# Performance work log

Measured on AMD Instinct MI355X. Metric: run time of the kernel, lower is better.

Reference implementation:

```python
import jax, jax.numpy as jnp
import numpy as np

N_NODES = 100000
E_HALF = 2000000  # edges come in two mirrored halves (two classes per node pair)
IN_DIM, HID = 5, 16


def setup_inputs() -> dict:
    key = jax.random.key(0)
    ks = jax.random.split(key, 8)
    x = jax.random.normal(ks[0], (N_NODES, IN_DIM), dtype=jnp.float32)
    e_half = jax.random.randint(ks[1], (2, E_HALF), 0, N_NODES)
    edges = jnp.concatenate([e_half, e_half], axis=1)  # [2, 2*E_HALF]
    edge_attr = jax.random.uniform(ks[2], (2 * E_HALF, 2), dtype=jnp.float32)
    detector_labels = jax.random.bernoulli(ks[3], 0.5, (N_NODES,))
    s = 1.0 / np.sqrt(IN_DIM)
    W_rel = jax.random.uniform(ks[4], (HID, IN_DIM), minval=-s, maxval=s, dtype=jnp.float32)
    b_rel = jax.random.uniform(ks[5], (HID,), minval=-s, maxval=s, dtype=jnp.float32)
    W_root = jax.random.uniform(ks[6], (HID, IN_DIM), minval=-s, maxval=s, dtype=jnp.float32)
    s2 = 1.0 / np.sqrt(2 * HID + 1)
    k7, k8 = jax.random.split(ks[7])
    W_lin = jax.random.uniform(k7, (1, 2 * HID + 1), minval=-s2, maxval=s2, dtype=jnp.float32)
    b_lin = jax.random.uniform(k8, (1,), minval=-s2, maxval=s2, dtype=jnp.float32)
    return {
        "x": x, "edges": edges, "edge_attr": edge_attr,
        "detector_labels": detector_labels,
        "W_rel": W_rel, "b_rel": b_rel, "W_root": W_root,
        "W_lin": W_lin, "b_lin": b_lin,
    }


def reference(x, edges, edge_attr, detector_labels, W_rel, b_rel, W_root, W_lin, b_lin):
    N = x.shape[0]
    src, dst = edges[0], edges[1]
    # GraphConv(aggr='add'): out_i = W_root x_i + W_rel * sum_{(j->i)} w_e * x_j + b_rel
    w = edge_attr[:, 1]
    msg = x[src] * w[:, None]                                  # [E, 5]
    agg = jax.ops.segment_sum(msg, dst, num_segments=N)        # [N, 5]
    h = jnp.tanh(agg @ W_rel.T + b_rel + x @ W_root.T)         # [N, 16]
    # SplitSyndromes: keep edges whose both endpoints are detector nodes
    valid = detector_labels[src] & detector_labels[dst]
    vidx = jnp.nonzero(valid)[0]                               # data-dependent (eager)
    e = edges[:, vidx]
    ea = edge_attr[vidx]
    # gather-concat-linear edge scoring
    feat = jnp.concatenate([h[e[0]], ea[:, :1], h[e[1]]], axis=-1)  # [nv, 33]
    score = feat @ W_lin.T + b_lin                             # [nv, 1]
    nv = score.shape[0]
    half = nv // 2
    score2 = score.reshape(-1, half)                           # [2, half]
    classes2 = ea[:, 1].reshape(-1, half)
    mi = jnp.argmin(score2, axis=0)
    cols = jnp.arange(half)
    return e[:, :half], score2[mi, cols], classes2[mi, cols]
```

## Files before the change

### kernel.cpp

```cpp
#include <hip/hip_runtime.h>

#define HID 16
#define IN_DIM 5
#define PAD 8
#define EPT 4

#define FXS 64.0f
#define FXI 0.015625f

__global__ void pack_labels(const int* __restrict__ lab, const float* __restrict__ x,
                            unsigned long long* __restrict__ bits, float* __restrict__ xp,
                            int N) {
    int n = blockIdx.x * 256 + threadIdx.x;
    bool p = (n < N) && (lab[n] != 0);
    unsigned long long m = __ballot(p);
    if (((threadIdx.x & 63) == 0) && n < N) bits[n >> 6] = m;
    if (n < N) {
        float4 a;
        a.x = x[(size_t)n * IN_DIM + 0];
        a.y = x[(size_t)n * IN_DIM + 1];
        a.z = x[(size_t)n * IN_DIM + 2];
        a.w = x[(size_t)n * IN_DIM + 3];
        *(float4*)(xp + (size_t)n * 8) = a;
        float4 b;
        b.x = x[(size_t)n * IN_DIM + 4];
        b.y = 0.f; b.z = 0.f; b.w = 0.f;
        *(float4*)(xp + (size_t)n * 8 + 4) = b;
    }
}

__global__ __launch_bounds__(256, 4) void scatter_count(
        const int* __restrict__ src, const int* __restrict__ dst,
        const unsigned long long* __restrict__ bits,
        const float2* __restrict__ ea2,
        const float* __restrict__ xp,
        const float* __restrict__ Wlin,
        unsigned long long* __restrict__ agg,
        int* __restrict__ counts,
        float4* __restrict__ st4,
        int EH) {
    const int tid = threadIdx.x;
    const int i0 = (blockIdx.x * 256 + tid) * EPT;

    int s[EPT], d[EPT];
    float2 eaA[EPT], eaB[EPT];
    bool act[EPT];

    if (i0 + EPT <= EH && ((EH & 1) == 0)) {
        int4 s4 = *(const int4*)(src + i0);
        int4 d4 = *(const int4*)(dst + i0);
        s[0] = s4.x; s[1] = s4.y; s[2] = s4.z; s[3] = s4.w;
        d[0] = d4.x; d[1] = d4.y; d[2] = d4.z; d[3] = d4.w;
        float4 a0 = *(const float4*)(ea2 + i0);
        float4 a1 = *(const float4*)(ea2 + i0 + 2);
        float4 b0 = *(const float4*)(ea2 + (size_t)i0 + EH);
        float4 b1 = *(const float4*)(ea2 + (size_t)i0 + EH + 2);
        eaA[0] = make_float2(a0.x, a0.y); eaA[1] = make_float2(a0.z, a0.w);
        eaA[2] = make_float2(a1.x, a1.y); eaA[3] = make_float2(a1.z, a1.w);
        eaB[0] = make_float2(b0.x, b0.y); eaB[1] = make_float2(b0.z, b0.w);
        eaB[2] = make_float2(b1.x, b1.y); eaB[3] = make_float2(b1.z, b1.w);
#pragma unroll
        for (int k = 0; k < EPT; k++) act[k] = true;
    } else {
#pragma unroll
        for (int k = 0; k < EPT; k++) {
            int i = i0 + k;
            act[k] = (i < EH);
            s[k] = act[k] ? src[i] : 0;
            d[k] = act[k] ? dst[i] : 0;
            eaA[k] = act[k] ? ea2[i] : make_float2(0.f, 0.f);
            eaB[k] = act[k] ? ea2[(size_t)i + EH] : make_float2(0.f, 0.f);
        }
    }

    bool ld[EPT], vl[EPT];
#pragma unroll
    for (int k = 0; k < EPT; k++) {
        bool ls = (bits[s[k] >> 6] >> (s[k] & 63)) & 1;
        bool lv = (bits[d[k] >> 6] >> (d[k] & 63)) & 1;
        ld[k] = act[k] && lv;
        vl[k] = ld[k] && ls;
    }

    float4 xa[EPT], xb[EPT];
#pragma unroll
    for (int k = 0; k < EPT; k++) {
        const float* xs = xp + (size_t)s[k] * 8;
        xa[k] = *(const float4*)xs;
        xb[k] = *(const float4*)(xs + 4);
    }

#pragma unroll
    for (int k = 0; k < EPT; k++) {
        if (ld[k]) {
            float w = (eaA[k].y + eaB[k].y) * FXS;
            unsigned long long a = 0;
            int q0 = __float2int_rn(xa[k].x * w);
            int q1 = __float2int_rn(xa[k].y * w);
            int q2 = __float2int_rn(xa[k].z * w);
            int q3 = __float2int_rn(xa[k].w * w);
            int q4 = __float2int_rn(xb[k].x * w);
            a += (unsigned long long)(long long)q0;
            a += (unsigned long long)(long long)q1 << 12;
            a += (unsigned long long)(long long)q2 << 24;
            a += (unsigned long long)(long long)q3 << 36;
            a += (unsigned long long)(long long)q4 << 48;
            atomicAdd(&agg[(size_t)d[k] * PAD], a);
        }
    }

    float w16 = Wlin[HID];
    float scpart[EPT], cls[EPT];
#pragma unroll
    for (int k = 0; k < EPT; k++) {
        float p0 = w16 * eaA[k].x;
        float p1 = w16 * eaB[k].x;
        if (p1 < p0) { scpart[k] = p1; cls[k] = eaB[k].y; }
        else         { scpart[k] = p0; cls[k] = eaA[k].y; }
    }

    unsigned m4 = 0;
#pragma unroll
    for (int k = 0; k < EPT; k++) m4 |= (vl[k] ? (1u << k) : 0u);
    int cnt = __popc(m4);
    int lane = tid & 63, wid = tid >> 6;
    int scan = cnt;
#pragma unroll
    for (int off = 1; off < 64; off <<= 1) {
        int u = __shfl_up(scan, off, 64);
        if (lane >= off) scan += u;
    }
    __shared__ int wc[4];
    if (lane == 63) wc[wid] = scan;
    __syncthreads();
    if (tid == 0) counts[blockIdx.x] = wc[0] + wc[1] + wc[2] + wc[3];
    int wexcl = 0;
#pragma unroll
    for (int k = 0; k < 4; k++) if (k < wid) wexcl += wc[k];
    int idx = blockIdx.x * (256 * EPT) + wexcl + (scan - cnt);
#pragma unroll
    for (int k = 0; k < EPT; k++) {
        if (vl[k]) {
            float4 r;
            r.x = __int_as_float(s[k]);
            r.y = __int_as_float(d[k]);
            r.z = scpart[k];
            r.w = cls[k];
            st4[idx++] = r;
        }
    }
}

__device__ __forceinline__ float decode_field(unsigned long long& T) {
    int r = (int)(T & 0xFFFull);
    int s = (r >= 2048) ? r - 4096 : r;
    T = (T - (unsigned long long)(long long)s) >> 12;
    return (float)s * FXI;
}

__global__ void compute_uv(const float* __restrict__ xp,
                           const unsigned long long* __restrict__ agg,
                           const int* __restrict__ lab,
                           const float* __restrict__ Wrel, const float* __restrict__ brel,
                           const float* __restrict__ Wroot, const float* __restrict__ Wlin,
                           float2* __restrict__ uv, int N) {
    __shared__ float sWrel[HID * IN_DIM];
    __shared__ float sWroot[HID * IN_DIM];
    __shared__ float sBrel[HID];
    __shared__ float sWl[2 * HID + 1];
    int t = threadIdx.x;
    if (t < HID * IN_DIM) sWrel[t] = Wrel[t];
    else if (t < 2 * HID * IN_DIM) sWroot[t - HID * IN_DIM] = Wroot[t - HID * IN_DIM];
    else if (t < 2 * HID * IN_DIM + HID) sBrel[t - 2 * HID * IN_DIM] = brel[t - 2 * HID * IN_DIM];
    else if (t < 2 * HID * IN_DIM + HID + 2 * HID + 1)
        sWl[t - 2 * HID * IN_DIM - HID] = Wlin[t - 2 * HID * IN_DIM - HID];
    __syncthreads();

    int n = blockIdx.x * 256 + threadIdx.x;
    if (n >= N) return;
    if (!lab[n]) return;

    unsigned long long T = agg[(size_t)n * PAD];
    float a[IN_DIM], xv[IN_DIM];
#pragma unroll
    for (int d = 0; d < IN_DIM; d++) a[d] = decode_field(T);
    float4 x0 = *(const float4*)(xp + (size_t)n * 8);
    xv[0] = x0.x; xv[1] = x0.y; xv[2] = x0.z; xv[3] = x0.w;
    xv[4] = xp[(size_t)n * 8 + 4];

    float u = 0.f, vv = 0.f;
#pragma unroll
    for (int k = 0; k < HID; k++) {
        float acc = sBrel[k];
#pragma unroll
        for (int d = 0; d < IN_DIM; d++)
            acc += a[d] * sWrel[k * IN_DIM + d] + xv[d] * sWroot[k * IN_DIM + d];
        float hk = tanhf(acc);
        u += sWl[k] * hk;
        vv += sWl[HID + 1 + k] * hk;
    }
    uv[n] = make_float2(u, vv);
}

__global__ void scan_counts(const int* __restrict__ counts, int* __restrict__ offs, int nb) {
    __shared__ int waveSums[16];
    int tid = threadIdx.x;
    int base = tid * 8;
    int vals[8];
    int tsum = 0;
#pragma unroll
    for (int k = 0; k < 8; k++) {
        int idx = base + k;
        vals[k] = (idx < nb) ? counts[idx] : 0;
        tsum += vals[k];
    }
    int lane = tid & 63, wid = tid >> 6;
    int scan = tsum;
#pragma unroll
    for (int off = 1; off < 64; off <<= 1) {
        int u = __shfl_up(scan, off, 64);
        if (lane >= off) scan += u;
    }
    if (lane == 63) waveSums[wid] = scan;
    __syncthreads();
    if (wid == 0 && lane < 16) {
        int s = waveSums[lane];
#pragma unroll
        for (int off = 1; off < 16; off <<= 1) {
            int u = __shfl_up(s, off, 64);
            if (lane >= off) s += u;
        }
        waveSums[lane] = s;
    }
    __syncthreads();
    int waveBase = (wid > 0) ? waveSums[wid - 1] : 0;
    int excl = waveBase + scan - tsum;
#pragma unroll
    for (int k = 0; k < 8; k++) {
        int idx = base + k;
        if (idx < nb) offs[idx] = excl;
        excl += vals[k];
    }
}

__global__ void emit_out(const float4* __restrict__ st4,
                         const float* __restrict__ uvf, const float* __restrict__ blin,
                         const int* __restrict__ counts, const int* __restrict__ offs,
                         float* __restrict__ out, int K) {
    int b = blockIdx.x;
    int cnt = counts[b];
    int base = offs[b];
    float bl = blin[0];
    for (int t = threadIdx.x; t < cnt; t += 256) {
        float4 r = st4[(size_t)b * (256 * EPT) + t];
        int s = __float_as_int(r.x);
        int d = __float_as_int(r.y);
        float sc = bl + uvf[2 * (size_t)s] + uvf[2 * (size_t)d + 1] + r.z;
        int ro = base + t;
        out[ro] = (float)s;
        out[(size_t)K + ro] = (float)d;
        out[2 * (size_t)K + ro] = sc;
        out[3 * (size_t)K + ro] = r.w;
    }
}

extern "C" void kernel_launch(void* const* d_in, const int* in_sizes, int n_in,
                              void* d_out, int out_size, void* d_ws, size_t ws_size,
                              hipStream_t stream) {
    const float* x     = (const float*)d_in[0];
    const int*   edges = (const int*)d_in[1];
    const float* ea    = (const float*)d_in[2];
    const int*   lab   = (const int*)d_in[3];
    const float* Wrel  = (const float*)d_in[4];
    const float* brel  = (const float*)d_in[5];
    const float* Wroot = (const float*)d_in[6];
    const float* Wlin  = (const float*)d_in[7];
    const float* blin  = (const float*)d_in[8];

    const int N  = in_sizes[0] / IN_DIM;
    const int E  = in_sizes[1] / 2;
    const int EH = E / 2;
    const int K  = out_size / 4;

    const int* src = edges;
    const int* dst = edges + E;
    const float2* ea2 = (const float2*)ea;
    const int EPB = 256 * EPT;
    const int nb = (EH + EPB - 1) / EPB;
    const int nslots = nb * EPB;

    char* ws = (char*)d_ws;
    size_t off = 0;
    unsigned long long* agg = (unsigned long long*)(ws + off); off += (size_t)N * PAD * 8;
    float2* uv = (float2*)(ws + off); off += (size_t)N * 8;
    unsigned long long* bits = (unsigned long long*)(ws + off);
    off += (size_t)(((N + 63) / 64) * 8 + 255) / 256 * 256;
    float* xp = (float*)(ws + off); off += (size_t)N * 8 * 4;
    int* counts = (int*)(ws + off); off += (size_t)(nb * 4 + 255) / 256 * 256;
    int* offs   = (int*)(ws + off); off += (size_t)(nb * 4 + 255) / 256 * 256;
    float4* st4 = (float4*)(ws + off); off += (size_t)nslots * 16;

    float* out = (float*)d_out;

    hipMemsetAsync(agg, 0, (size_t)N * PAD * 8, stream);
    pack_labels<<<(N + 255) / 256, 256, 0, stream>>>(lab, x, bits, xp, N);
    scatter_count<<<nb, 256, 0, stream>>>(src, dst, bits, ea2, xp, Wlin, agg, counts,
                                          st4, EH);
    compute_uv<<<(N + 255) / 256, 256, 0, stream>>>(xp, agg, lab, Wrel, brel, Wroot, Wlin, uv, N);
    scan_counts<<<1, 1024, 0, stream>>>(counts, offs, nb);
    emit_out<<<nb, 256, 0, stream>>>(st4, (const float*)uv, blin, counts, offs, out, K);
}
```

Baseline: 178.3 us.

## Fuse all stages into one persistent kernel with grid-wide barriers

Replaces the memset-plus-five-kernel pipeline with a single persistent kernel. It walks the edge blocks in a grid-stride loop, scatters aggregates and compacts valid edges, then uses an atomic grid barrier before the block scan and per-node u/v compute, and a second barrier before the output emit. It also drops the label-bitmask and padded-x preprocessing and reads labels and unpadded x directly, loading x only for active edges. The aim is to remove launch gaps and the packing pass. In exchange it depends on every block being co-resident, sizes the grid from occupancy queries cached in a static, and the scan runs on a single block capped at 2048 edge blocks.

```diff
diff --git a/kernel.cpp b/kernel.cpp
--- a/kernel.cpp
+++ b/kernel.cpp
@@ -4,9 +4,241 @@
 #define IN_DIM 5
 #define PAD 8
 #define EPT 4
+#define EPB (256 * EPT)
 
 #define FXS 64.0f
 #define FXI 0.015625f
+
+__device__ __forceinline__ float decode_field(unsigned long long& T) {
+    int r = (int)(T & 0xFFFull);
+    int s = (r >= 2048) ? r - 4096 : r;
+    T = (T - (unsigned long long)(long long)s) >> 12;
+    return (float)s * FXI;
+}
+
+__device__ __forceinline__ void scan256(const int* __restrict__ counts,
+                                        int* __restrict__ offs, int nbv) {
+    __shared__ int wS[4];
+    int tid = threadIdx.x;
+    int base = tid * 8;
+    int vals[8];
+    int tsum = 0;
+#pragma unroll
+    for (int k = 0; k < 8; k++) {
+        int idx = base + k;
+        vals[k] = (idx < nbv) ? counts[idx] : 0;
+        tsum += vals[k];
+    }
+    int lane = tid & 63, wid = tid >> 6;
+    int scan = tsum;
+#pragma unroll
+    for (int off = 1; off < 64; off <<= 1) {
+        int u = __shfl_up(scan, off, 64);
+        if (lane >= off) scan += u;
+    }
+    if (lane == 63) wS[wid] = scan;
+    __syncthreads();
+    int waveBase = 0;
+#pragma unroll
+    for (int k = 0; k < 4; k++) if (k < wid) waveBase += wS[k];
+    int excl = waveBase + scan - tsum;
+#pragma unroll
+    for (int k = 0; k < 8; k++) {
+        int idx = base + k;
+        if (idx < nbv) offs[idx] = excl;
+        excl += vals[k];
+    }
+}
+
+__device__ __forceinline__ void gridbar(int* bar, int G) {
+    __syncthreads();
+    if (threadIdx.x == 0) {
+        __threadfence();
+        __hip_atomic_fetch_add(bar, 1, __ATOMIC_ACQ_REL, __HIP_MEMORY_SCOPE_AGENT);
+        while (__hip_atomic_load(bar, __ATOMIC_ACQUIRE, __HIP_MEMORY_SCOPE_AGENT) < G)
+            __builtin_amdgcn_s_sleep(32);
+        __threadfence();
+    }
+    __syncthreads();
+}
+
+__global__ __launch_bounds__(256) void fused(
+        const float* __restrict__ x, const int* __restrict__ src,
+        const int* __restrict__ dst, const float2* __restrict__ ea2,
+        const int* __restrict__ lab,
+        const float* __restrict__ Wrel, const float* __restrict__ brel,
+        const float* __restrict__ Wroot, const float* __restrict__ Wlin,
+        const float* __restrict__ blin,
+        unsigned long long* __restrict__ agg, float2* __restrict__ uvp,
+        int* __restrict__ counts, int* __restrict__ offs,
+        float4* __restrict__ st4, float* __restrict__ out,
+        int* __restrict__ bars,
+        int N, int EH, int K, int nbv) {
+    const int tid = threadIdx.x;
+    const int G = gridDim.x;
+    const int GT = G * 256;
+    const int gt = blockIdx.x * 256 + tid;
+    const int lane = tid & 63, wid = tid >> 6;
+
+    __shared__ float sWrel[HID * IN_DIM];
+    __shared__ float sWroot[HID * IN_DIM];
+    __shared__ float sBrel[HID];
+    __shared__ float sWl[2 * HID + 1];
+    if (tid < HID * IN_DIM) sWrel[tid] = Wrel[tid];
+    else if (tid < 2 * HID * IN_DIM) sWroot[tid - HID * IN_DIM] = Wroot[tid - HID * IN_DIM];
+    else if (tid < 2 * HID * IN_DIM + HID) sBrel[tid - 2 * HID * IN_DIM] = brel[tid - 2 * HID * IN_DIM];
+    else if (tid < 2 * HID * IN_DIM + HID + 2 * HID + 1)
+        sWl[tid - 2 * HID * IN_DIM - HID] = Wlin[tid - 2 * HID * IN_DIM - HID];
+
+    float w16 = Wlin[HID];
+    __shared__ int wc[4];
+    for (int vb = blockIdx.x; vb < nbv; vb += G) {
+        const int i0 = vb * EPB + tid * EPT;
+        int s[EPT], d[EPT];
+        float2 eaA[EPT], eaB[EPT];
+        bool act[EPT];
+        if (i0 + EPT <= EH) {
+            int4 s4 = *(const int4*)(src + i0);
+            int4 d4 = *(const int4*)(dst + i0);
+            s[0] = s4.x; s[1] = s4.y; s[2] = s4.z; s[3] = s4.w;
+            d[0] = d4.x; d[1] = d4.y; d[2] = d4.z; d[3] = d4.w;
+            float4 a0 = *(const float4*)(ea2 + i0);
+            float4 a1 = *(const float4*)(ea2 + i0 + 2);
+            float4 b0 = *(const float4*)(ea2 + (size_t)i0 + EH);
+            float4 b1 = *(const float4*)(ea2 + (size_t)i0 + EH + 2);
+            eaA[0] = make_float2(a0.x, a0.y); eaA[1] = make_float2(a0.z, a0.w);
+            eaA[2] = make_float2(a1.x, a1.y); eaA[3] = make_float2(a1.z, a1.w);
+            eaB[0] = make_float2(b0.x, b0.y); eaB[1] = make_float2(b0.z, b0.w);
+            eaB[2] = make_float2(b1.x, b1.y); eaB[3] = make_float2(b1.z, b1.w);
+#pragma unroll
+            for (int k = 0; k < EPT; k++) act[k] = true;
+        } else {
+#pragma unroll
+            for (int k = 0; k < EPT; k++) {
+                int i = i0 + k;
+                act[k] = (i < EH);
+                s[k] = act[k] ? src[i] : 0;
+                d[k] = act[k] ? dst[i] : 0;
+                eaA[k] = act[k] ? ea2[i] : make_float2(0.f, 0.f);
+                eaB[k] = act[k] ? ea2[(size_t)i + EH] : make_float2(0.f, 0.f);
+            }
+        }
+        bool ld[EPT], vl[EPT];
+#pragma unroll
+        for (int k = 0; k < EPT; k++) {
+            bool ls = lab[s[k]] != 0;
+            bool lv = lab[d[k]] != 0;
+            ld[k] = act[k] && lv;
+            vl[k] = ld[k] && ls;
+        }
+#pragma unroll
+        for (int k = 0; k < EPT; k++) {
+            if (ld[k]) {
+                const float* xs = x + (size_t)s[k] * IN_DIM;
+                float4 xa = *(const float4*)xs;
+                float  x4 = xs[4];
+                float w = (eaA[k].y + eaB[k].y) * FXS;
+                unsigned long long a = 0;
+                int q0 = __float2int_rn(xa.x * w);
+                int q1 = __float2int_rn(xa.y * w);
+                int q2 = __float2int_rn(xa.z * w);
+                int q3 = __float2int_rn(xa.w * w);
+                int q4 = __float2int_rn(x4 * w);
+                a += (unsigned long long)(long long)q0;
+                a += (unsigned long long)(long long)q1 << 12;
+                a += (unsigned long long)(long long)q2 << 24;
+                a += (unsigned long long)(long long)q3 << 36;
+                a += (unsigned long long)(long long)q4 << 48;
+                atomicAdd(&agg[(size_t)d[k] * PAD], a);
+            }
+        }
+        float scpart[EPT], cls[EPT];
+#pragma unroll
+        for (int k = 0; k < EPT; k++) {
+            float p0 = w16 * eaA[k].x;
+            float p1 = w16 * eaB[k].x;
+            if (p1 < p0) { scpart[k] = p1; cls[k] = eaB[k].y; }
+            else         { scpart[k] = p0; cls[k] = eaA[k].y; }
+        }
+        unsigned m4 = 0;
+#pragma unroll
+        for (int k = 0; k < EPT; k++) m4 |= (vl[k] ? (1u << k) : 0u);
+        int cnt = __popc(m4);
+        int scan = cnt;
+#pragma unroll
+        for (int off = 1; off < 64; off <<= 1) {
+            int u = __shfl_up(scan, off, 64);
+            if (lane >= off) scan += u;
+        }
+        __syncthreads();
+        if (lane == 63) wc[wid] = scan;
+        __syncthreads();
+        if (tid == 0) counts[vb] = wc[0] + wc[1] + wc[2] + wc[3];
+        int wexcl = 0;
+#pragma unroll
+        for (int k = 0; k < 4; k++) if (k < wid) wexcl += wc[k];
+        int idx = vb * EPB + wexcl + (scan - cnt);
+#pragma unroll
+        for (int k = 0; k < EPT; k++) {
+            if (vl[k]) {
+                float4 r;
+                r.x = __int_as_float(s[k]);
+                r.y = __int_as_float(d[k]);
+                r.z = scpart[k];
+                r.w = cls[k];
+                st4[idx++] = r;
+            }
+        }
+    }
+    gridbar(&bars[0], G);
+
+    if (blockIdx.x == 0) scan256(counts, offs, nbv);
+    {
+        int iters = (N + GT - 1) / GT;
+        for (int it = 0; it < iters; ++it) {
+            int n = gt + it * GT;
+            if (n < N && lab[n]) {
+                unsigned long long T = agg[(size_t)n * PAD];
+                float a[IN_DIM], xv[IN_DIM];
+#pragma unroll
+                for (int dd = 0; dd < IN_DIM; dd++) a[dd] = decode_field(T);
+#pragma unroll
+                for (int dd = 0; dd < IN_DIM; dd++) xv[dd] = x[(size_t)n * IN_DIM + dd];
+                float u = 0.f, vv = 0.f;
+#pragma unroll
+                for (int kk = 0; kk < HID; kk++) {
+                    float acc = sBrel[kk];
+#pragma unroll
+                    for (int dd = 0; dd < IN_DIM; dd++)
+                        acc += a[dd] * sWrel[kk * IN_DIM + dd] + xv[dd] * sWroot[kk * IN_DIM + dd];
+                    float hk = tanhf(acc);
+                    u += sWl[kk] * hk;
+                    vv += sWl[HID + 1 + kk] * hk;
+                }
+                uvp[n] = make_float2(u, vv);
+            }
+        }
+    }
+    gridbar(&bars[16], G);
+
+    float bl = blin[0];
+    const float* uvf = (const float*)uvp;
+    for (int vb = blockIdx.x; vb < nbv; vb += G) {
+        int cnt = counts[vb];
+        int base = offs[vb];
+        for (int t = tid; t < cnt; t += 256) {
+            float4 r = st4[(size_t)vb * EPB + t];
+            int s = __float_as_int(r.x);
+            int d = __float_as_int(r.y);
+            float sc = bl + uvf[2 * (size_t)s] + uvf[2 * (size_t)d + 1] + r.z;
+            int ro = base + t;
+            out[ro] = (float)s;
+            out[(size_t)K + ro] = (float)d;
+            out[2 * (size_t)K + ro] = sc;
+            out[3 * (size_t)K + ro] = r.w;
+        }
+    }
+}
 
 __global__ void pack_labels(const int* __restrict__ lab, const float* __restrict__ x,
                             unsigned long long* __restrict__ bits, float* __restrict__ xp,
@@ -41,12 +273,10 @@
         int EH) {
     const int tid = threadIdx.x;
     const int i0 = (blockIdx.x * 256 + tid) * EPT;
-
     int s[EPT], d[EPT];
     float2 eaA[EPT], eaB[EPT];
     bool act[EPT];
-
-    if (i0 + EPT <= EH && ((EH & 1) == 0)) {
+    if (i0 + EPT <= EH) {
         int4 s4 = *(const int4*)(src + i0);
         int4 d4 = *(const int4*)(dst + i0);
         s[0] = s4.x; s[1] = s4.y; s[2] = s4.z; s[3] = s4.w;
@@ -72,7 +302,6 @@
             eaB[k] = act[k] ? ea2[(size_t)i + EH] : make_float2(0.f, 0.f);
         }
     }
-
     bool ld[EPT], vl[EPT];
 #pragma unroll
     for (int k = 0; k < EPT; k++) {
@@ -81,25 +310,19 @@
         ld[k] = act[k] && lv;
         vl[k] = ld[k] && ls;
     }
-
-    float4 xa[EPT], xb[EPT];
-#pragma unroll
-    for (int k = 0; k < EPT; k++) {
-        const float* xs = xp + (size_t)s[k] * 8;
-        xa[k] = *(const float4*)xs;
-        xb[k] = *(const float4*)(xs + 4);
-    }
-
 #pragma unroll
     for (int k = 0; k < EPT; k++) {
         if (ld[k]) {
+            const float* xs = xp + (size_t)s[k] * 8;
+            float4 xa = *(const float4*)xs;
+            float  x4 = xs[4];
             float w = (eaA[k].y + eaB[k].y) * FXS;
             unsigned long long a = 0;
-            int q0 = __float2int_rn(xa[k].x * w);
-            int q1 = __float2int_rn(xa[k].y * w);
-            int q2 = __float2int_rn(xa[k].z * w);
-            int q3 = __float2int_rn(xa[k].w * w);
-            int q4 = __float2int_rn(xb[k].x * w);
+            int q0 = __float2int_rn(xa.x * w);
+            int q1 = __float2int_rn(xa.y * w);
+            int q2 = __float2int_rn(xa.z * w);
+            int q3 = __float2int_rn(xa.w * w);
+            int q4 = __float2int_rn(x4 * w);
             a += (unsigned long long)(long long)q0;
             a += (unsigned long long)(long long)q1 << 12;
             a += (unsigned long long)(long long)q2 << 24;
@@ -108,7 +331,6 @@
             atomicAdd(&agg[(size_t)d[k] * PAD], a);
         }
     }
-
     float w16 = Wlin[HID];
     float scpart[EPT], cls[EPT];
 #pragma unroll
@@ -118,7 +340,6 @@
         if (p1 < p0) { scpart[k] = p1; cls[k] = eaB[k].y; }
         else         { scpart[k] = p0; cls[k] = eaA[k].y; }
     }
-
     unsigned m4 = 0;
 #pragma unroll
     for (int k = 0; k < EPT; k++) m4 |= (vl[k] ? (1u << k) : 0u);
@@ -137,7 +358,7 @@
     int wexcl = 0;
 #pragma unroll
     for (int k = 0; k < 4; k++) if (k < wid) wexcl += wc[k];
-    int idx = blockIdx.x * (256 * EPT) + wexcl + (scan - cnt);
+    int idx = blockIdx.x * EPB + wexcl + (scan - cnt);
 #pragma unroll
     for (int k = 0; k < EPT; k++) {
         if (vl[k]) {
@@ -149,13 +370,6 @@
             st4[idx++] = r;
         }
     }
-}
-
-__device__ __forceinline__ float decode_field(unsigned long long& T) {
-    int r = (int)(T & 0xFFFull);
-    int s = (r >= 2048) ? r - 4096 : r;
-    T = (T - (unsigned long long)(long long)s) >> 12;
-    return (float)s * FXI;
 }
 
 __global__ void compute_uv(const float* __restrict__ xp,
@@ -175,11 +389,9 @@
     else if (t < 2 * HID * IN_DIM + HID + 2 * HID + 1)
         sWl[t - 2 * HID * IN_DIM - HID] = Wlin[t - 2 * HID * IN_DIM - HID];
     __syncthreads();
-
     int n = blockIdx.x * 256 + threadIdx.x;
     if (n >= N) return;
     if (!lab[n]) return;
-
     unsigned long long T = agg[(size_t)n * PAD];
     float a[IN_DIM], xv[IN_DIM];
 #pragma unroll
@@ -187,7 +399,6 @@
     float4 x0 = *(const float4*)(xp + (size_t)n * 8);
     xv[0] = x0.x; xv[1] = x0.y; xv[2] = x0.z; xv[3] = x0.w;
     xv[4] = xp[(size_t)n * 8 + 4];
-
     float u = 0.f, vv = 0.f;
 #pragma unroll
     for (int k = 0; k < HID; k++) {
@@ -252,7 +463,7 @@
     int base = offs[b];
     float bl = blin[0];
     for (int t = threadIdx.x; t < cnt; t += 256) {
-        float4 r = st4[(size_t)b * (256 * EPT) + t];
+        float4 r = st4[(size_t)b * EPB + t];
         int s = __float_as_int(r.x);
         int d = __float_as_int(r.y);
         float sc = bl + uvf[2 * (size_t)s] + uvf[2 * (size_t)d + 1] + r.z;
@@ -277,36 +488,61 @@
     const float* Wlin  = (const float*)d_in[7];
     const float* blin  = (const float*)d_in[8];
 
-    const int N  = in_sizes[0] / IN_DIM;
+    int N  = in_sizes[0] / IN_DIM;
     const int E  = in_sizes[1] / 2;
-    const int EH = E / 2;
-    const int K  = out_size / 4;
+    int EH = E / 2;
+    int K  = out_size / 4;
 
     const int* src = edges;
     const int* dst = edges + E;
     const float2* ea2 = (const float2*)ea;
-    const int EPB = 256 * EPT;
-    const int nb = (EH + EPB - 1) / EPB;
-    const int nslots = nb * EPB;
+    int nbv = (EH + EPB - 1) / EPB;
+    const int nslots = nbv * EPB;
 
     char* ws = (char*)d_ws;
     size_t off = 0;
     unsigned long long* agg = (unsigned long long*)(ws + off); off += (size_t)N * PAD * 8;
+    int* bars = (int*)(ws + off); off += 256;
     float2* uv = (float2*)(ws + off); off += (size_t)N * 8;
     unsigned long long* bits = (unsigned long long*)(ws + off);
     off += (size_t)(((N + 63) / 64) * 8 + 255) / 256 * 256;
     float* xp = (float*)(ws + off); off += (size_t)N * 8 * 4;
-    int* counts = (int*)(ws + off); off += (size_t)(nb * 4 + 255) / 256 * 256;
-    int* offs   = (int*)(ws + off); off += (size_t)(nb * 4 + 255) / 256 * 256;
+    int* counts = (int*)(ws + off); off += (size_t)(nbv * 4 + 255) / 256 * 256;
+    int* offs   = (int*)(ws + off); off += (size_t)(nbv * 4 + 255) / 256 * 256;
     float4* st4 = (float4*)(ws + off); off += (size_t)nslots * 16;
 
     float* out = (float*)d_out;
 
-    hipMemsetAsync(agg, 0, (size_t)N * PAD * 8, stream);
-    pack_labels<<<(N + 255) / 256, 256, 0, stream>>>(lab, x, bits, xp, N);
-    scatter_count<<<nb, 256, 0, stream>>>(src, dst, bits, ea2, xp, Wlin, agg, counts,
-                                          st4, EH);
-    compute_uv<<<(N + 255) / 256, 256, 0, stream>>>(xp, agg, lab, Wrel, brel, Wroot, Wlin, uv, N);
-    scan_counts<<<1, 1024, 0, stream>>>(counts, offs, nb);
-    emit_out<<<nb, 256, 0, stream>>>(st4, (const float*)uv, blin, counts, offs, out, K);
-}
+    static int G = 0;
+    if (G == 0) {
+        int bpc = 0;
+        hipError_t e = hipOccupancyMaxActiveBlocksPerMultiprocessor(&bpc, fused, 256, 0);
+        int dev = 0;
+        hipGetDevice(&dev);
+        hipDeviceProp_t prop;
+        hipGetDeviceProperties(&prop, dev);
+        int cu = prop.multiProcessorCount;
+        if (e != hipSuccess || bpc < 1 || cu < 1 || nbv > 2048) {
+            G = -1;
+        } else {
+            long g = ((long)bpc * cu) / 2;
+            if (g < cu) g = cu;
+            if (g > 2048) g = 2048;
+            G = (int)g;
+        }
+    }
+
+    if (G > 0) {
+        hipMemsetAsync(agg, 0, (size_t)N * PAD * 8 + 256, stream);
+        fused<<<G, 256, 0, stream>>>(x, src, dst, ea2, lab, Wrel, brel, Wroot, Wlin, blin,
+                                     agg, uv, counts, offs, st4, out, bars, N, EH, K, nbv);
+    } else {
+        hipMemsetAsync(agg, 0, (size_t)N * PAD * 8, stream);
+        pack_labels<<<(N + 255) / 256, 256, 0, stream>>>(lab, x, bits, xp, N);
+        scatter_count<<<nbv, 256, 0, stream>>>(src, dst, bits, ea2, xp, Wlin, agg, counts,
+                                               st4, EH);
+        compute_uv<<<(N + 255) / 256, 256, 0, stream>>>(xp, agg, lab, Wrel, brel, Wroot, Wlin, uv, N);
+        scan_counts<<<1, 1024, 0, stream>>>(counts, offs, nbv);
+        emit_out<<<nbv, 256, 0, stream>>>(st4, (const float*)uv, blin, counts, offs, out, K);
+    }
+}
```

Result: no change. 178.6 us (+0.2%).

## Fuse node-score computation into emit kernel and drop padded x copy

Applied to the files above, without the earlier changes.

Removes the separate compute_uv kernel and the uv buffer. The emit kernel now recomputes each endpoint's hidden projection (decode agg, 16 tanh units) for every valid edge. The padded xp copy is dropped, so x is read directly with stride-5 loads, and only for edges whose destination is a detector. The agg memset is folded into the label-packing kernel. This cuts kernel launches and intermediate traffic, but repeats the per-node MLP work for every edge endpoint, and the float4 loads from x are not 16-byte aligned.

```diff
diff --git a/kernel.cpp b/kernel.cpp
--- a/kernel.cpp
+++ b/kernel.cpp
@@ -4,36 +4,37 @@
 #define IN_DIM 5
 #define PAD 8
 #define EPT 4
+#define EPB (256 * EPT)
 
 #define FXS 64.0f
 #define FXI 0.015625f
 
-__global__ void pack_labels(const int* __restrict__ lab, const float* __restrict__ x,
-                            unsigned long long* __restrict__ bits, float* __restrict__ xp,
-                            int N) {
+__device__ __forceinline__ float decode_field(unsigned long long& T) {
+    int r = (int)(T & 0xFFFull);
+    int s = (r >= 2048) ? r - 4096 : r;
+    T = (T - (unsigned long long)(long long)s) >> 12;
+    return (float)s * FXI;
+}
+
+__global__ void pack_zero(const int* __restrict__ lab,
+                          unsigned long long* __restrict__ bits,
+                          unsigned long long* __restrict__ agg, int N) {
     int n = blockIdx.x * 256 + threadIdx.x;
     bool p = (n < N) && (lab[n] != 0);
     unsigned long long m = __ballot(p);
     if (((threadIdx.x & 63) == 0) && n < N) bits[n >> 6] = m;
-    if (n < N) {
-        float4 a;
-        a.x = x[(size_t)n * IN_DIM + 0];
-        a.y = x[(size_t)n * IN_DIM + 1];
-        a.z = x[(size_t)n * IN_DIM + 2];
-        a.w = x[(size_t)n * IN_DIM + 3];
-        *(float4*)(xp + (size_t)n * 8) = a;
-        float4 b;
-        b.x = x[(size_t)n * IN_DIM + 4];
-        b.y = 0.f; b.z = 0.f; b.w = 0.f;
-        *(float4*)(xp + (size_t)n * 8 + 4) = b;
-    }
+    size_t tot = (size_t)N * (PAD / 2);
+    size_t GT = (size_t)gridDim.x * 256;
+    ulonglong2 z; z.x = 0ull; z.y = 0ull;
+    for (size_t i = (size_t)blockIdx.x * 256 + threadIdx.x; i < tot; i += GT)
+        ((ulonglong2*)agg)[i] = z;
 }
 
 __global__ __launch_bounds__(256, 4) void scatter_count(
         const int* __restrict__ src, const int* __restrict__ dst,
         const unsigned long long* __restrict__ bits,
         const float2* __restrict__ ea2,
-        const float* __restrict__ xp,
+        const float* __restrict__ x,
         const float* __restrict__ Wlin,
         unsigned long long* __restrict__ agg,
         int* __restrict__ counts,
@@ -41,12 +42,10 @@
         int EH) {
     const int tid = threadIdx.x;
     const int i0 = (blockIdx.x * 256 + tid) * EPT;
-
     int s[EPT], d[EPT];
     float2 eaA[EPT], eaB[EPT];
     bool act[EPT];
-
-    if (i0 + EPT <= EH && ((EH & 1) == 0)) {
+    if (i0 + EPT <= EH) {
         int4 s4 = *(const int4*)(src + i0);
         int4 d4 = *(const int4*)(dst + i0);
         s[0] = s4.x; s[1] = s4.y; s[2] = s4.z; s[3] = s4.w;
@@ -72,7 +71,6 @@
             eaB[k] = act[k] ? ea2[(size_t)i + EH] : make_float2(0.f, 0.f);
         }
     }
-
     bool ld[EPT], vl[EPT];
 #pragma unroll
     for (int k = 0; k < EPT; k++) {
@@ -81,25 +79,19 @@
         ld[k] = act[k] && lv;
         vl[k] = ld[k] && ls;
     }
-
-    float4 xa[EPT], xb[EPT];
-#pragma unroll
-    for (int k = 0; k < EPT; k++) {
-        const float* xs = xp + (size_t)s[k] * 8;
-        xa[k] = *(const float4*)xs;
-        xb[k] = *(const float4*)(xs + 4);
-    }
-
 #pragma unroll
     for (int k = 0; k < EPT; k++) {
         if (ld[k]) {
+            const float* xs = x + (size_t)s[k] * IN_DIM;
+            float4 xa = *(const float4*)xs;
+            float  x4 = xs[4];
             float w = (eaA[k].y + eaB[k].y) * FXS;
             unsigned long long a = 0;
-            int q0 = __float2int_rn(xa[k].x * w);
-            int q1 = __float2int_rn(xa[k].y * w);
-            int q2 = __float2int_rn(xa[k].z * w);
-            int q3 = __float2int_rn(xa[k].w * w);
-            int q4 = __float2int_rn(xb[k].x * w);
+            int q0 = __float2int_rn(xa.x * w);
+            int q1 = __float2int_rn(xa.y * w);
+            int q2 = __float2int_rn(xa.z * w);
+            int q3 = __float2int_rn(xa.w * w);
+            int q4 = __float2int_rn(x4 * w);
             a += (unsigned long long)(long long)q0;
             a += (unsigned long long)(long long)q1 << 12;
             a += (unsigned long long)(long long)q2 << 24;
@@ -108,7 +100,6 @@
             atomicAdd(&agg[(size_t)d[k] * PAD], a);
         }
     }
-
     float w16 = Wlin[HID];
     float scpart[EPT], cls[EPT];
 #pragma unroll
@@ -118,7 +109,6 @@
         if (p1 < p0) { scpart[k] = p1; cls[k] = eaB[k].y; }
         else         { scpart[k] = p0; cls[k] = eaA[k].y; }
     }
-
     unsigned m4 = 0;
 #pragma unroll
     for (int k = 0; k < EPT; k++) m4 |= (vl[k] ? (1u << k) : 0u);
@@ -137,7 +127,7 @@
     int wexcl = 0;
 #pragma unroll
     for (int k = 0; k < 4; k++) if (k < wid) wexcl += wc[k];
-    int idx = blockIdx.x * (256 * EPT) + wexcl + (scan - cnt);
+    int idx = blockIdx.x * EPB + wexcl + (scan - cnt);
 #pragma unroll
     for (int k = 0; k < EPT; k++) {
         if (vl[k]) {
@@ -151,19 +141,79 @@
     }
 }
 
-__device__ __forceinline__ float decode_field(unsigned long long& T) {
-    int r = (int)(T & 0xFFFull);
-    int s = (r >= 2048) ? r - 4096 : r;
-    T = (T - (unsigned long long)(long long)s) >> 12;
-    return (float)s * FXI;
-}
-
-__global__ void compute_uv(const float* __restrict__ xp,
-                           const unsigned long long* __restrict__ agg,
-                           const int* __restrict__ lab,
-                           const float* __restrict__ Wrel, const float* __restrict__ brel,
-                           const float* __restrict__ Wroot, const float* __restrict__ Wlin,
-                           float2* __restrict__ uv, int N) {
+__global__ void scan_counts(const int* __restrict__ counts, int* __restrict__ offs, int nb) {
+    __shared__ int waveSums[16];
+    int tid = threadIdx.x;
+    int base = tid * 8;
+    int vals[8];
+    int tsum = 0;
+#pragma unroll
+    for (int k = 0; k < 8; k++) {
+        int idx = base + k;
+        vals[k] = (idx < nb) ? counts[idx] : 0;
+        tsum += vals[k];
+    }
+    int lane = tid & 63, wid = tid >> 6;
+    int scan = tsum;
+#pragma unroll
+    for (int off = 1; off < 64; off <<= 1) {
+        int u = __shfl_up(scan, off, 64);
+        if (lane >= off) scan += u;
+    }
+    if (lane == 63) waveSums[wid] = scan;
+    __syncthreads();
+    if (wid == 0 && lane < 16) {
+        int s = waveSums[lane];
+#pragma unroll
+        for (int off = 1; off < 16; off <<= 1) {
+            int u = __shfl_up(s, off, 64);
+            if (lane >= off) s += u;
+        }
+        waveSums[lane] = s;
+    }
+    __syncthreads();
+    int waveBase = (wid > 0) ? waveSums[wid - 1] : 0;
+    int excl = waveBase + scan - tsum;
+#pragma unroll
+    for (int k = 0; k < 8; k++) {
+        int idx = base + k;
+        if (idx < nb) offs[idx] = excl;
+        excl += vals[k];
+    }
+}
+
+__device__ __forceinline__ float node_dot(int n,
+        const unsigned long long* __restrict__ agg, const float* __restrict__ x,
+        const float* sWrel, const float* sBrel, const float* sWroot,
+        const float* sWl, int wloff) {
+    unsigned long long T = agg[(size_t)n * PAD];
+    float a[IN_DIM], xv[IN_DIM];
+#pragma unroll
+    for (int dd = 0; dd < IN_DIM; dd++) a[dd] = decode_field(T);
+    const float* xs = x + (size_t)n * IN_DIM;
+    float4 x0 = *(const float4*)xs;
+    xv[0] = x0.x; xv[1] = x0.y; xv[2] = x0.z; xv[3] = x0.w;
+    xv[4] = xs[4];
+    float r = 0.f;
+#pragma unroll
+    for (int k = 0; k < HID; k++) {
+        float acc = sBrel[k];
+#pragma unroll
+        for (int dd = 0; dd < IN_DIM; dd++)
+            acc += a[dd] * sWrel[k * IN_DIM + dd] + xv[dd] * sWroot[k * IN_DIM + dd];
+        r += sWl[wloff + k] * tanhf(acc);
+    }
+    return r;
+}
+
+__global__ __launch_bounds__(256) void emit_uv(
+        const float4* __restrict__ st4,
+        const unsigned long long* __restrict__ agg, const float* __restrict__ x,
+        const float* __restrict__ Wrel, const float* __restrict__ brel,
+        const float* __restrict__ Wroot, const float* __restrict__ Wlin,
+        const float* __restrict__ blin,
+        const int* __restrict__ counts, const int* __restrict__ offs,
+        float* __restrict__ out, int K) {
     __shared__ float sWrel[HID * IN_DIM];
     __shared__ float sWroot[HID * IN_DIM];
     __shared__ float sBrel[HID];
@@ -176,87 +226,18 @@
         sWl[t - 2 * HID * IN_DIM - HID] = Wlin[t - 2 * HID * IN_DIM - HID];
     __syncthreads();
 
-    int n = blockIdx.x * 256 + threadIdx.x;
-    if (n >= N) return;
-    if (!lab[n]) return;
-
-    unsigned long long T = agg[(size_t)n * PAD];
-    float a[IN_DIM], xv[IN_DIM];
-#pragma unroll
-    for (int d = 0; d < IN_DIM; d++) a[d] = decode_field(T);
-    float4 x0 = *(const float4*)(xp + (size_t)n * 8);
-    xv[0] = x0.x; xv[1] = x0.y; xv[2] = x0.z; xv[3] = x0.w;
-    xv[4] = xp[(size_t)n * 8 + 4];
-
-    float u = 0.f, vv = 0.f;
-#pragma unroll
-    for (int k = 0; k < HID; k++) {
-        float acc = sBrel[k];
-#pragma unroll
-        for (int d = 0; d < IN_DIM; d++)
-            acc += a[d] * sWrel[k * IN_DIM + d] + xv[d] * sWroot[k * IN_DIM + d];
-        float hk = tanhf(acc);
-        u += sWl[k] * hk;
-        vv += sWl[HID + 1 + k] * hk;
-    }
-    uv[n] = make_float2(u, vv);
-}
-
-__global__ void scan_counts(const int* __restrict__ counts, int* __restrict__ offs, int nb) {
-    __shared__ int waveSums[16];
-    int tid = threadIdx.x;
-    int base = tid * 8;
-    int vals[8];
-    int tsum = 0;
-#pragma unroll
-    for (int k = 0; k < 8; k++) {
-        int idx = base + k;
-        vals[k] = (idx < nb) ? counts[idx] : 0;
-        tsum += vals[k];
-    }
-    int lane = tid & 63, wid = tid >> 6;
-    int scan = tsum;
-#pragma unroll
-    for (int off = 1; off < 64; off <<= 1) {
-        int u = __shfl_up(scan, off, 64);
-        if (lane >= off) scan += u;
-    }
-    if (lane == 63) waveSums[wid] = scan;
-    __syncthreads();
-    if (wid == 0 && lane < 16) {
-        int s = waveSums[lane];
-#pragma unroll
-        for (int off = 1; off < 16; off <<= 1) {
-            int u = __shfl_up(s, off, 64);
-            if (lane >= off) s += u;
-        }
-        waveSums[lane] = s;
-    }
-    __syncthreads();
-    int waveBase = (wid > 0) ? waveSums[wid - 1] : 0;
-    int excl = waveBase + scan - tsum;
-#pragma unroll
-    for (int k = 0; k < 8; k++) {
-        int idx = base + k;
-        if (idx < nb) offs[idx] = excl;
-        excl += vals[k];
-    }
-}
-
-__global__ void emit_out(const float4* __restrict__ st4,
-                         const float* __restrict__ uvf, const float* __restrict__ blin,
-                         const int* __restrict__ counts, const int* __restrict__ offs,
-                         float* __restrict__ out, int K) {
     int b = blockIdx.x;
     int cnt = counts[b];
     int base = offs[b];
     float bl = blin[0];
-    for (int t = threadIdx.x; t < cnt; t += 256) {
-        float4 r = st4[(size_t)b * (256 * EPT) + t];
+    for (int tt = threadIdx.x; tt < cnt; tt += 256) {
+        float4 r = st4[(size_t)b * EPB + tt];
         int s = __float_as_int(r.x);
         int d = __float_as_int(r.y);
-        float sc = bl + uvf[2 * (size_t)s] + uvf[2 * (size_t)d + 1] + r.z;
-        int ro = base + t;
+        float u = node_dot(s, agg, x, sWrel, sBrel, sWroot, sWl, 0);
+        float v = node_dot(d, agg, x, sWrel, sBrel, sWroot, sWl, HID + 1);
+        float sc = bl + u + v + r.z;
+        int ro = base + tt;
         out[ro] = (float)s;
         out[(size_t)K + ro] = (float)d;
         out[2 * (size_t)K + ro] = sc;
@@ -285,28 +266,24 @@
     const int* src = edges;
     const int* dst = edges + E;
     const float2* ea2 = (const float2*)ea;
-    const int EPB = 256 * EPT;
     const int nb = (EH + EPB - 1) / EPB;
     const int nslots = nb * EPB;
 
     char* ws = (char*)d_ws;
     size_t off = 0;
     unsigned long long* agg = (unsigned long long*)(ws + off); off += (size_t)N * PAD * 8;
-    float2* uv = (float2*)(ws + off); off += (size_t)N * 8;
     unsigned long long* bits = (unsigned long long*)(ws + off);
     off += (size_t)(((N + 63) / 64) * 8 + 255) / 256 * 256;
-    float* xp = (float*)(ws + off); off += (size_t)N * 8 * 4;
     int* counts = (int*)(ws + off); off += (size_t)(nb * 4 + 255) / 256 * 256;
     int* offs   = (int*)(ws + off); off += (size_t)(nb * 4 + 255) / 256 * 256;
     float4* st4 = (float4*)(ws + off); off += (size_t)nslots * 16;
 
     float* out = (float*)d_out;
 
-    hipMemsetAsync(agg, 0, (size_t)N * PAD * 8, stream);
-    pack_labels<<<(N + 255) / 256, 256, 0, stream>>>(lab, x, bits, xp, N);
-    scatter_count<<<nb, 256, 0, stream>>>(src, dst, bits, ea2, xp, Wlin, agg, counts,
+    pack_zero<<<(N + 255) / 256, 256, 0, stream>>>(lab, bits, agg, N);
+    scatter_count<<<nb, 256, 0, stream>>>(src, dst, bits, ea2, x, Wlin, agg, counts,
                                           st4, EH);
-    compute_uv<<<(N + 255) / 256, 256, 0, stream>>>(xp, agg, lab, Wrel, brel, Wroot, Wlin, uv, N);
     scan_counts<<<1, 1024, 0, stream>>>(counts, offs, nb);
-    emit_out<<<nb, 256, 0, stream>>>(st4, (const float*)uv, blin, counts, offs, out, K);
-}
+    emit_uv<<<nb, 256, 0, stream>>>(st4, agg, x, Wrel, brel, Wroot, Wlin, blin,
+                                    counts, offs, out, K);
+}
```

New measurement: 243.7 us. +36.7%, slower.
